# Performance work log

Hardware: AMD Instinct MI355X
Metric: run time of the kernel (lower is better)

Reference implementation:

```python
import jax, jax.numpy as jnp
import numpy as np


def setup_inputs() -> dict:
    key = jax.random.key(0)
    k1, k2, k3 = jax.random.split(key, 3)
    N, DIN, DOUT = 8192, 256, 256
    adjacency = jax.random.uniform(k1, (N, N), dtype=jnp.float32)
    input_feature = jax.random.normal(k2, (N, DIN), dtype=jnp.float32)
    weight = jax.random.normal(k3, (DIN, DOUT), dtype=jnp.float32) * (1.0 / np.sqrt(DIN))
    bias = jnp.zeros((DOUT,), dtype=jnp.float32)
    return {"adjacency": adjacency, "input_feature": input_feature,
            "weight": weight, "bias": bias, "l": 1}


def reference(adjacency, input_feature, weight, bias, l):
    # support = X @ W
    support = input_feature @ weight  # [N, DOUT]
    # A = adjacency + l*I ; degrees = rowsum(A) = rowsum(adjacency) + l
    deg = jnp.sum(adjacency, axis=1) + jnp.asarray(l, adjacency.dtype)  # [N]
    # D^{-1/2} with inf (from zero degree) replaced by 0
    d = jnp.where(deg > 0, deg ** -0.5, jnp.zeros_like(deg))  # [N]
    # D @ adjacency @ D  (row scale then col scale of the ORIGINAL adjacency,
    # self-loops only affect the degree, matching the torch code)
    norm_adj = adjacency * d[:, None] * d[None, :]  # [N, N]
    out = norm_adj @ support + bias  # [N, DOUT]
    return out
```

## Files before the change

### kernel.cpp

```cpp
#include <hip/hip_runtime.h>


typedef __attribute__((ext_vector_type(8))) short short8;
typedef __attribute__((ext_vector_type(4))) float f32x4;

#define NN 8192
#define DD 256
#define KCHUNK 2048
#define BK 64
#define NITER (KCHUNK / BK)

__device__ inline unsigned short f2bfu(float x) {
    unsigned int u = __builtin_bit_cast(unsigned int, x);
    u += 0x7fffu + ((u >> 16) & 1u);
    return (unsigned short)(u >> 16);
}
__device__ inline unsigned int f2bf2u(float x, float y) {
    return (unsigned int)f2bfu(x) | ((unsigned int)f2bfu(y) << 16);
}
__device__ inline short8 cvt8(float4 a, float4 b) {
    union { unsigned int i[4]; short8 s; } u;
    u.i[0] = f2bf2u(a.x, a.y);
    u.i[1] = f2bf2u(a.z, a.w);
    u.i[2] = f2bf2u(b.x, b.y);
    u.i[3] = f2bf2u(b.z, b.w);
    return u.s;
}

__device__ inline void gload16(const void* g, void* l) {
    __builtin_amdgcn_global_load_lds(
        (const __attribute__((address_space(1))) unsigned int*)g,
        (__attribute__((address_space(3))) unsigned int*)l, 16, 0, 0);
}

#define BLOAD(dst, ptr, OFFSTR)                                        \
    asm volatile("global_load_dwordx4 %0, %1, off offset:" OFFSTR      \
                 : "=v"(dst) : "v"(ptr))

__global__ __launch_bounds__(256) void rowsum_conv(const float* __restrict__ A,
                                                   const int* __restrict__ lp,
                                                   float* __restrict__ d,
                                                   unsigned short* __restrict__ Abf) {
    const int t = threadIdx.x;
    const int rl = t >> 4;
    const int cg = t & 15;
    const int i = blockIdx.x * 16 + rl;
    const int ti = i >> 6;
    const int rt = i & 63;
    const int swz = (rt & 7) << 4;

    const f32x4* Ar = (const f32x4*)(A + (size_t)i * NN);
    char* tb = (char*)Abf + (size_t)ti * 128 * 8192 + rt * 128 + ((8 * cg) ^ swz);

    float s0 = 0.f, s1 = 0.f;
#pragma unroll 4
    for (int k = 0; k < 128; ++k) {
        f32x4 v = __builtin_nontemporal_load(Ar + cg + 16 * k);
        s0 += v[0] + v[1];
        s1 += v[2] + v[3];
        *(uint2*)(tb + (size_t)k * 8192) =
            make_uint2(f2bf2u(v[0], v[1]), f2bf2u(v[2], v[3]));
    }
    float s = s0 + s1;
#pragma unroll
    for (int off = 8; off > 0; off >>= 1) s += __shfl_down(s, off, 16);
    if (cg == 0) {
        float deg = s + (float)(*lp);
        d[i] = deg > 0.f ? rsqrtf(deg) : 0.f;
    }
}

__global__ __launch_bounds__(256) void wtrans_kernel(const float* __restrict__ W,
                                                     unsigned short* __restrict__ WT) {
    __shared__ unsigned short tile[64][65];
    const int tx = threadIdx.x & 63, ty = threadIdx.x >> 6;
    const int i0 = (blockIdx.x & 3) * 64;
    const int n0 = (blockIdx.x >> 2) * 64;
#pragma unroll
    for (int r = ty; r < 64; r += 4)
        tile[r][tx] = f2bfu(W[(size_t)(i0 + r) * DD + n0 + tx]);
    __syncthreads();
#pragma unroll
    for (int r = ty; r < 64; r += 4)
        WT[(size_t)(n0 + r) * DD + i0 + tx] = tile[tx][r];
}

__global__ __launch_bounds__(256) void support_kernel(const float* __restrict__ X,
                                                      const unsigned short* __restrict__ WT,
                                                      const float* __restrict__ d,
                                                      unsigned short* __restrict__ ST) {
    const int j0 = blockIdx.x * 16;
    const int lane = threadIdx.x & 63;
    const int w = threadIdx.x >> 6;
    const int q = lane >> 4;
    const int l15 = lane & 15;
    const int nb = w * 64;

    f32x4 acc[4];
#pragma unroll
    for (int b = 0; b < 4; ++b) acc[b] = (f32x4)(0.f);

    const float* Xbase = X + (size_t)(j0 + l15) * DD + q * 8;
    const unsigned short* Wbase = WT + (size_t)(nb + l15) * DD + q * 8;

#pragma unroll
    for (int k0 = 0; k0 < DD; k0 += 32) {
        const float4* p = (const float4*)(Xbase + k0);
        short8 afr = cvt8(p[0], p[1]);
        short8 bfr[4];
#pragma unroll
        for (int ni = 0; ni < 4; ++ni)
            bfr[ni] = *(const short8*)(Wbase + ni * 16 * DD + k0);
#pragma unroll
        for (int ni = 0; ni < 4; ++ni)
            acc[ni] = __builtin_amdgcn_mfma_f32_16x16x32_bf16(afr, bfr[ni], acc[ni], 0, 0, 0);
    }

    const int j0r = j0 + q * 4;
    float dj[4];
#pragma unroll
    for (int r = 0; r < 4; ++r) dj[r] = d[j0r + r];
    const int ktile = j0r >> 6;
    const int kk2i = (j0r >> 5) & 1;
    const int qi = (j0r >> 3) & 3;
    const int bo = (j0r & 7) * 2;
#pragma unroll
    for (int ni = 0; ni < 4; ++ni) {
        const int n = nb + ni * 16 + l15;
        unsigned int lo = f2bf2u(acc[ni][0] * dj[0], acc[ni][1] * dj[1]);
        unsigned int hi = f2bf2u(acc[ni][2] * dj[2], acc[ni][3] * dj[3]);
        char* dst = (char*)ST + (size_t)(n >> 5) * 524288 + ktile * 4096 +
                    kk2i * 2048 + ((n >> 4) & 1) * 1024 + (qi * 16 + (n & 15)) * 16 + bo;
        *(uint2*)dst = make_uint2(lo, hi);
    }
}

__global__ __launch_bounds__(512, 4) void main_gemm(const unsigned short* __restrict__ Abf,
                                                    const unsigned short* __restrict__ ST,
                                                    float* __restrict__ part) {
    __shared__ __align__(16) unsigned short Abuf[4][4096];

    const int bid = blockIdx.x;
    const int kc = (bid & 7) >> 1;
    const int mt = ((bid >> 3) << 1) | (bid & 1);
    const int tid = threadIdx.x;
    const int lane = tid & 63;
    const int w = tid >> 6;
    const int q = lane >> 4;
    const int l15 = lane & 15;
    const int swz = (l15 & 7) << 4;

    const char* Ag = (const char*)Abf + ((size_t)mt * 128 + kc * NITER) * 8192 + tid * 16;

    const char* Pb = (const char*)ST + (size_t)w * 524288 + (size_t)kc * 32 * 4096 + lane * 16;

    f32x4 acc[4][2];
#pragma unroll
    for (int a = 0; a < 4; ++a)
#pragma unroll
        for (int b = 0; b < 2; ++b) acc[a][b] = (f32x4)(0.f);

    short8 bfr[2][2][2];

    gload16(Ag, (char*)&Abuf[0][0] + tid * 16);
    __builtin_amdgcn_sched_barrier(0);
    BLOAD(bfr[0][0][0], Pb, "0");
    BLOAD(bfr[0][0][1], Pb, "1024");
    BLOAD(bfr[0][1][0], Pb, "2048");
    BLOAD(bfr[0][1][1], Pb, "3072");
    __builtin_amdgcn_sched_barrier(0);
    gload16(Ag + 8192, (char*)&Abuf[1][0] + tid * 16);
    __builtin_amdgcn_sched_barrier(0);
    {
        const char* Pb1 = Pb + 4096;
        BLOAD(bfr[1][0][0], Pb1, "0");
        BLOAD(bfr[1][0][1], Pb1, "1024");
        BLOAD(bfr[1][1][0], Pb1, "2048");
        BLOAD(bfr[1][1][1], Pb1, "3072");
    }
    __builtin_amdgcn_sched_barrier(0);

    const char* AbBase = (const char*)&Abuf[0][0] + l15 * 128;
    const char* PbN = Pb + 8192;

#pragma unroll 2
    for (int it = 0; it < NITER - 2; ++it) {
        __asm__ __volatile__("s_waitcnt vmcnt(5)\n\ts_barrier" ::: "memory");
        __builtin_amdgcn_sched_barrier(0);

        gload16(Ag + (size_t)(it + 2) * 8192,
                (char*)&Abuf[0][0] + (((it + 2) & 3) << 13) + tid * 16);
        __builtin_amdgcn_sched_barrier(0);

        const char* Ab = AbBase + ((it & 3) << 13);
#pragma unroll
        for (int kk2 = 0; kk2 < 2; ++kk2) {
            short8 afr[4];
#pragma unroll
            for (int mi = 0; mi < 4; ++mi)
                afr[mi] = *(const short8*)(Ab + mi * 2048 + ((kk2 * 64 + q * 16) ^ swz));
#pragma unroll
            for (int mi = 0; mi < 4; ++mi)
#pragma unroll
                for (int ni = 0; ni < 2; ++ni)
                    acc[mi][ni] = __builtin_amdgcn_mfma_f32_16x16x32_bf16(
                        afr[mi], bfr[it & 1][kk2][ni], acc[mi][ni], 0, 0, 0);
        }
        __builtin_amdgcn_sched_barrier(0);

        BLOAD(bfr[it & 1][0][0], PbN, "0");
        BLOAD(bfr[it & 1][0][1], PbN, "1024");
        BLOAD(bfr[it & 1][1][0], PbN, "2048");
        BLOAD(bfr[it & 1][1][1], PbN, "3072");
        PbN += 4096;
        __builtin_amdgcn_sched_barrier(0);
    }

    __asm__ __volatile__("s_waitcnt vmcnt(5)\n\ts_barrier" ::: "memory");
    __builtin_amdgcn_sched_barrier(0);
    {
        const char* Ab = AbBase + (((NITER - 2) & 3) << 13);
#pragma unroll
        for (int kk2 = 0; kk2 < 2; ++kk2) {
            short8 afr[4];
#pragma unroll
            for (int mi = 0; mi < 4; ++mi)
                afr[mi] = *(const short8*)(Ab + mi * 2048 + ((kk2 * 64 + q * 16) ^ swz));
#pragma unroll
            for (int mi = 0; mi < 4; ++mi)
#pragma unroll
                for (int ni = 0; ni < 2; ++ni)
                    acc[mi][ni] = __builtin_amdgcn_mfma_f32_16x16x32_bf16(
                        afr[mi], bfr[0][kk2][ni], acc[mi][ni], 0, 0, 0);
        }
    }
    __asm__ __volatile__("s_waitcnt vmcnt(0)\n\ts_barrier" ::: "memory");
    __builtin_amdgcn_sched_barrier(0);
    {
        const char* Ab = AbBase + (((NITER - 1) & 3) << 13);
#pragma unroll
        for (int kk2 = 0; kk2 < 2; ++kk2) {
            short8 afr[4];
#pragma unroll
            for (int mi = 0; mi < 4; ++mi)
                afr[mi] = *(const short8*)(Ab + mi * 2048 + ((kk2 * 64 + q * 16) ^ swz));
#pragma unroll
            for (int mi = 0; mi < 4; ++mi)
#pragma unroll
                for (int ni = 0; ni < 2; ++ni)
                    acc[mi][ni] = __builtin_amdgcn_mfma_f32_16x16x32_bf16(
                        afr[mi], bfr[1][kk2][ni], acc[mi][ni], 0, 0, 0);
        }
    }

    float* P = part + (size_t)kc * NN * DD;
#pragma unroll
    for (int mi = 0; mi < 4; ++mi) {
        const int r0 = mt * 64 + mi * 16 + q * 4;
#pragma unroll
        for (int ni = 0; ni < 2; ++ni) {
            const int n = w * 32 + ni * 16 + l15;
#pragma unroll
            for (int rr = 0; rr < 4; ++rr)
                P[(size_t)(r0 + rr) * DD + n] = acc[mi][ni][rr];
        }
    }
}

__global__ __launch_bounds__(256) void reduce_kernel(const float* __restrict__ part,
                                                     const float* __restrict__ d,
                                                     const float* __restrict__ bias,
                                                     float* __restrict__ out) {
    const int idx = blockIdx.x * 256 + threadIdx.x;
    const int i = idx >> 6;
    const int c4 = (idx & 63) << 2;
    const size_t off = (size_t)i * DD + c4;
    const size_t stride = (size_t)NN * DD;
    f32x4 s = *(const f32x4*)(part + off);
    s += *(const f32x4*)(part + stride + off);
    s += *(const f32x4*)(part + 2 * stride + off);
    s += *(const f32x4*)(part + 3 * stride + off);
    const float di = d[i];
    const f32x4 b = *(const f32x4*)(bias + c4);
    s = s * di + b;
    *(f32x4*)(out + off) = s;
}

extern "C" void kernel_launch(void* const* d_in, const int* in_sizes, int n_in,
                              void* d_out, int out_size, void* d_ws, size_t ws_size,
                              hipStream_t stream) {
    const float* A = (const float*)d_in[0];
    const float* X = (const float*)d_in[1];
    const float* W = (const float*)d_in[2];
    const float* bias = (const float*)d_in[3];
    const int* lp = (const int*)d_in[4];
    float* out = (float*)d_out;

    float* d = (float*)d_ws;
    unsigned short* WT = (unsigned short*)((char*)d_ws + 32768);
    unsigned short* ST = (unsigned short*)((char*)d_ws + 32768 + 131072);
    float* part = (float*)((char*)d_ws + 4358144);
    unsigned short* Abf = (unsigned short*)((char*)d_ws + 37912576);
    (void)ws_size;

    rowsum_conv<<<NN / 16, 256, 0, stream>>>(A, lp, d, Abf);
    wtrans_kernel<<<16, 256, 0, stream>>>(W, WT);
    support_kernel<<<NN / 16, 256, 0, stream>>>(X, WT, d, ST);
    main_gemm<<<128 * (NN / KCHUNK), 512, 0, stream>>>(Abf, ST, part);
    reduce_kernel<<<NN * DD / 4 / 256, 256, 0, stream>>>(part, d, bias, out);
}
```

Baseline: 446.1 us.

## Enlarge main GEMM block tile to 128 rows with 2x4 wave grid

Each main_gemm block now covers 128 rows instead of 64, arranged as a 2x4 wave grid where each wave computes 64x64 instead of 64x32. The grid is halved to 256 blocks, the LDS A buffer is doubled, and the waitcnt depth is raised to match the doubled load count. This is meant to raise MFMA work per B-fragment load and cut redundant global traffic for the support matrix. In exchange it uses more registers and LDS, lowers the occupancy target to 2, and leaves fewer blocks to spread across CUs.

```diff
diff --git a/kernel.cpp b/kernel.cpp
--- a/kernel.cpp
+++ b/kernel.cpp
@@ -135,10 +135,10 @@
     }
 }
 
-__global__ __launch_bounds__(512, 4) void main_gemm(const unsigned short* __restrict__ Abf,
+__global__ __launch_bounds__(512, 2) void main_gemm(const unsigned short* __restrict__ Abf,
                                                     const unsigned short* __restrict__ ST,
                                                     float* __restrict__ part) {
-    __shared__ __align__(16) unsigned short Abuf[4][4096];
+    __shared__ __align__(16) unsigned short Abuf[4][8192];
 
     const int bid = blockIdx.x;
     const int kc = (bid & 7) >> 1;
@@ -146,53 +146,73 @@
     const int tid = threadIdx.x;
     const int lane = tid & 63;
     const int w = tid >> 6;
+    const int wm = w >> 2;
+    const int wn = w & 3;
     const int q = lane >> 4;
     const int l15 = lane & 15;
     const int swz = (l15 & 7) << 4;
 
-    const char* Ag = (const char*)Abf + ((size_t)mt * 128 + kc * NITER) * 8192 + tid * 16;
-
-    const char* Pb = (const char*)ST + (size_t)w * 524288 + (size_t)kc * 32 * 4096 + lane * 16;
-
-    f32x4 acc[4][2];
+    const char* Ag0 = (const char*)Abf + ((size_t)(2 * mt) * 128 + kc * NITER) * 8192 + tid * 16;
+    const char* Ag1 = Ag0 + (size_t)128 * 8192;
+
+    const char* Pb0 = (const char*)ST + (size_t)(2 * wn) * 524288 + (size_t)kc * 32 * 4096 + lane * 16;
+    const char* Pb1 = Pb0 + 524288;
+
+    f32x4 acc[4][4];
 #pragma unroll
     for (int a = 0; a < 4; ++a)
 #pragma unroll
-        for (int b = 0; b < 2; ++b) acc[a][b] = (f32x4)(0.f);
-
-    short8 bfr[2][2][2];
-
-    gload16(Ag, (char*)&Abuf[0][0] + tid * 16);
-    __builtin_amdgcn_sched_barrier(0);
-    BLOAD(bfr[0][0][0], Pb, "0");
-    BLOAD(bfr[0][0][1], Pb, "1024");
-    BLOAD(bfr[0][1][0], Pb, "2048");
-    BLOAD(bfr[0][1][1], Pb, "3072");
-    __builtin_amdgcn_sched_barrier(0);
-    gload16(Ag + 8192, (char*)&Abuf[1][0] + tid * 16);
+        for (int b = 0; b < 4; ++b) acc[a][b] = (f32x4)(0.f);
+
+    short8 bfr[2][2][4];
+
+    gload16(Ag0, (char*)&Abuf[0][0] + tid * 16);
+    gload16(Ag1, (char*)&Abuf[0][0] + 8192 + tid * 16);
+    __builtin_amdgcn_sched_barrier(0);
+    BLOAD(bfr[0][0][0], Pb0, "0");
+    BLOAD(bfr[0][0][1], Pb0, "1024");
+    BLOAD(bfr[0][1][0], Pb0, "2048");
+    BLOAD(bfr[0][1][1], Pb0, "3072");
+    BLOAD(bfr[0][0][2], Pb1, "0");
+    BLOAD(bfr[0][0][3], Pb1, "1024");
+    BLOAD(bfr[0][1][2], Pb1, "2048");
+    BLOAD(bfr[0][1][3], Pb1, "3072");
+    __builtin_amdgcn_sched_barrier(0);
+    gload16(Ag0 + 8192, (char*)&Abuf[1][0] + tid * 16);
+    gload16(Ag1 + 8192, (char*)&Abuf[1][0] + 8192 + tid * 16);
     __builtin_amdgcn_sched_barrier(0);
     {
-        const char* Pb1 = Pb + 4096;
-        BLOAD(bfr[1][0][0], Pb1, "0");
-        BLOAD(bfr[1][0][1], Pb1, "1024");
-        BLOAD(bfr[1][1][0], Pb1, "2048");
-        BLOAD(bfr[1][1][1], Pb1, "3072");
-    }
-    __builtin_amdgcn_sched_barrier(0);
-
-    const char* AbBase = (const char*)&Abuf[0][0] + l15 * 128;
-    const char* PbN = Pb + 8192;
+        const char* Qb0 = Pb0 + 4096;
+        const char* Qb1 = Pb1 + 4096;
+        BLOAD(bfr[1][0][0], Qb0, "0");
+        BLOAD(bfr[1][0][1], Qb0, "1024");
+        BLOAD(bfr[1][1][0], Qb0, "2048");
+        BLOAD(bfr[1][1][1], Qb0, "3072");
+        BLOAD(bfr[1][0][2], Qb1, "0");
+        BLOAD(bfr[1][0][3], Qb1, "1024");
+        BLOAD(bfr[1][1][2], Qb1, "2048");
+        BLOAD(bfr[1][1][3], Qb1, "3072");
+    }
+    __builtin_amdgcn_sched_barrier(0);
+
+    const char* AbBase = (const char*)&Abuf[0][0] + wm * 8192 + l15 * 128;
+    const char* PbN0 = Pb0 + 8192;
+    const char* PbN1 = Pb1 + 8192;
 
 #pragma unroll 2
     for (int it = 0; it < NITER - 2; ++it) {
-        __asm__ __volatile__("s_waitcnt vmcnt(5)\n\ts_barrier" ::: "memory");
+        __asm__ __volatile__("s_waitcnt vmcnt(10)\n\ts_barrier" ::: "memory");
         __builtin_amdgcn_sched_barrier(0);
 
-        gload16(Ag + (size_t)(it + 2) * 8192,
-                (char*)&Abuf[0][0] + (((it + 2) & 3) << 13) + tid * 16);
+        {
+            const size_t go = (size_t)(it + 2) * 8192;
+            char* ls = (char*)&Abuf[0][0] + (((it + 2) & 3) << 14) + tid * 16;
+            gload16(Ag0 + go, ls);
+            gload16(Ag1 + go, ls + 8192);
+        }
         __builtin_amdgcn_sched_barrier(0);
 
-        const char* Ab = AbBase + ((it & 3) << 13);
+        const char* Ab = AbBase + ((it & 3) << 14);
 #pragma unroll
         for (int kk2 = 0; kk2 < 2; ++kk2) {
             short8 afr[4];
@@ -202,24 +222,29 @@
 #pragma unroll
             for (int mi = 0; mi < 4; ++mi)
 #pragma unroll
-                for (int ni = 0; ni < 2; ++ni)
+                for (int ni = 0; ni < 4; ++ni)
                     acc[mi][ni] = __builtin_amdgcn_mfma_f32_16x16x32_bf16(
                         afr[mi], bfr[it & 1][kk2][ni], acc[mi][ni], 0, 0, 0);
         }
         __builtin_amdgcn_sched_barrier(0);
 
-        BLOAD(bfr[it & 1][0][0], PbN, "0");
-        BLOAD(bfr[it & 1][0][1], PbN, "1024");
-        BLOAD(bfr[it & 1][1][0], PbN, "2048");
-        BLOAD(bfr[it & 1][1][1], PbN, "3072");
-        PbN += 4096;
+        BLOAD(bfr[it & 1][0][0], PbN0, "0");
+        BLOAD(bfr[it & 1][0][1], PbN0, "1024");
+        BLOAD(bfr[it & 1][1][0], PbN0, "2048");
+        BLOAD(bfr[it & 1][1][1], PbN0, "3072");
+        BLOAD(bfr[it & 1][0][2], PbN1, "0");
+        BLOAD(bfr[it & 1][0][3], PbN1, "1024");
+        BLOAD(bfr[it & 1][1][2], PbN1, "2048");
+        BLOAD(bfr[it & 1][1][3], PbN1, "3072");
+        PbN0 += 4096;
+        PbN1 += 4096;
         __builtin_amdgcn_sched_barrier(0);
     }
 
-    __asm__ __volatile__("s_waitcnt vmcnt(5)\n\ts_barrier" ::: "memory");
+    __asm__ __volatile__("s_waitcnt vmcnt(10)\n\ts_barrier" ::: "memory");
     __builtin_amdgcn_sched_barrier(0);
     {
-        const char* Ab = AbBase + (((NITER - 2) & 3) << 13);
+        const char* Ab = AbBase + (((NITER - 2) & 3) << 14);
 #pragma unroll
         for (int kk2 = 0; kk2 < 2; ++kk2) {
             short8 afr[4];
@@ -229,7 +254,7 @@
 #pragma unroll
             for (int mi = 0; mi < 4; ++mi)
 #pragma unroll
-                for (int ni = 0; ni < 2; ++ni)
+                for (int ni = 0; ni < 4; ++ni)
                     acc[mi][ni] = __builtin_amdgcn_mfma_f32_16x16x32_bf16(
                         afr[mi], bfr[0][kk2][ni], acc[mi][ni], 0, 0, 0);
         }
@@ -237,7 +262,7 @@
     __asm__ __volatile__("s_waitcnt vmcnt(0)\n\ts_barrier" ::: "memory");
     __builtin_amdgcn_sched_barrier(0);
     {
-        const char* Ab = AbBase + (((NITER - 1) & 3) << 13);
+        const char* Ab = AbBase + (((NITER - 1) & 3) << 14);
 #pragma unroll
         for (int kk2 = 0; kk2 < 2; ++kk2) {
             short8 afr[4];
@@ -247,7 +272,7 @@
 #pragma unroll
             for (int mi = 0; mi < 4; ++mi)
 #pragma unroll
-                for (int ni = 0; ni < 2; ++ni)
+                for (int ni = 0; ni < 4; ++ni)
                     acc[mi][ni] = __builtin_amdgcn_mfma_f32_16x16x32_bf16(
                         afr[mi], bfr[1][kk2][ni], acc[mi][ni], 0, 0, 0);
         }
@@ -256,10 +281,10 @@
     float* P = part + (size_t)kc * NN * DD;
 #pragma unroll
     for (int mi = 0; mi < 4; ++mi) {
-        const int r0 = mt * 64 + mi * 16 + q * 4;
-#pragma unroll
-        for (int ni = 0; ni < 2; ++ni) {
-            const int n = w * 32 + ni * 16 + l15;
+        const int r0 = mt * 128 + wm * 64 + mi * 16 + q * 4;
+#pragma unroll
+        for (int ni = 0; ni < 4; ++ni) {
+            const int n = wn * 64 + (ni >> 1) * 32 + (ni & 1) * 16 + l15;
 #pragma unroll
             for (int rr = 0; rr < 4; ++rr)
                 P[(size_t)(r0 + rr) * DD + n] = acc[mi][ni][rr];
@@ -306,6 +331,6 @@
     rowsum_conv<<<NN / 16, 256, 0, stream>>>(A, lp, d, Abf);
     wtrans_kernel<<<16, 256, 0, stream>>>(W, WT);
     support_kernel<<<NN / 16, 256, 0, stream>>>(X, WT, d, ST);
-    main_gemm<<<128 * (NN / KCHUNK), 512, 0, stream>>>(Abf, ST, part);
+    main_gemm<<<256, 512, 0, stream>>>(Abf, ST, part);
     reduce_kernel<<<NN * DD / 4 / 256, 256, 0, stream>>>(part, d, bias, out);
 }
```

Measured after the change: 438.5 us. Within noise of the previous version (-1.7%).
